# Performance work log

Measured on AMD Instinct MI355X. Metric: run time of the kernel, lower is better.

The kernel has to match this reference:

```python
import jax, jax.numpy as jnp
import numpy as np

D = 768      # hidden size (hardcoded in module)
H = 8        # MHA heads
DH = D // H  # head dim = 96
SLOPE = 0.01 # LeakyReLU default negative slope
NEG = -1e9


def _leaky(x):
    return jnp.where(x >= 0, x, SLOPE * x)


def setup_inputs() -> dict:
    key = jax.random.key(0)
    ks = jax.random.split(key, 20)
    B, S, T, C, L = 32, 2048, 64, 512, 16
    seq = jax.random.normal(ks[0], (B, S, D), dtype=jnp.float32)
    tab_ids = jax.random.randint(ks[1], (B, T, L), 0, S, dtype=jnp.int32)
    col_ids = jax.random.randint(ks[2], (B, C, L), 0, S, dtype=jnp.int32)
    # contiguous column->table assignment (8 cols/table), mirrors cumulative
    # slicing by column_number_in_each_table and keeps every table non-empty
    t_of_c = jnp.broadcast_to(jnp.repeat(jnp.arange(T, dtype=jnp.int32), C // T), (B, C))
    g = lambda k, sh: (jax.random.normal(k, sh, dtype=jnp.float32) * 0.02)
    return {
        "sequence_embeddings": seq,
        "table_token_ids": tab_ids,
        "column_token_ids": col_ids,
        "table_of_column": t_of_c,
        "W_tab_pool": g(ks[3], (D, D)), "b_tab_pool": g(ks[4], (D,)),
        "W_col_pool": g(ks[5], (D, D)), "b_col_pool": g(ks[6], (D,)),
        "in_proj_w": g(ks[7], (3 * D, D)), "in_proj_b": g(ks[8], (3 * D,)),
        "out_proj_w": g(ks[9], (D, D)), "out_proj_b": g(ks[10], (D,)),
        "W_t1": g(ks[11], (D, 256)), "b_t1": g(ks[12], (256,)),
        "W_t2": g(ks[13], (256, 2)), "b_t2": g(ks[14], (2,)),
        "W_c1": g(ks[15], (D, 256)), "b_c1": g(ks[16], (256,)),
        "W_c2": g(ks[17], (256, 2)), "b_c2": g(ks[18], (2,)),
    }


def reference(sequence_embeddings, table_token_ids, column_token_ids, table_of_column,
              W_tab_pool, b_tab_pool, W_col_pool, b_col_pool,
              in_proj_w, in_proj_b, out_proj_w, out_proj_b,
              W_t1, b_t1, W_t2, b_t2, W_c1, b_c1, W_c2, b_c2):
    B, T = table_token_ids.shape[:2]
    C = column_token_ids.shape[1]
    bi = jnp.arange(B)[:, None, None]
    # ragged span sum-pooling (gather + segment sum)
    tab = sequence_embeddings[bi, table_token_ids].sum(axis=2)   # [B,T,D]
    col = sequence_embeddings[bi, column_token_ids].sum(axis=2)  # [B,C,D]
    tab = _leaky(tab @ W_tab_pool + b_tab_pool)
    col = _leaky(col @ W_col_pool + b_col_pool)
    # per-table cross-attention (table query over its own columns), batched + masked
    Wq, Wk, Wv = jnp.split(in_proj_w, 3, axis=0)
    bq, bk, bv = jnp.split(in_proj_b, 3, axis=0)
    q = (tab @ Wq.T + bq).reshape(B, T, H, DH)
    k = (col @ Wk.T + bk).reshape(B, C, H, DH)
    v = (col @ Wv.T + bv).reshape(B, C, H, DH)
    scores = jnp.einsum('bthd,bchd->bhtc', q, k) / jnp.sqrt(jnp.float32(DH))
    mask = table_of_column[:, None, None, :] == jnp.arange(T, dtype=table_of_column.dtype)[None, None, :, None]
    attn = jax.nn.softmax(jnp.where(mask, scores, NEG), axis=-1)
    ctx = jnp.einsum('bhtc,bchd->bthd', attn, v).reshape(B, T, D)
    tab = tab + (ctx @ out_proj_w.T + out_proj_b)
    tab = tab / jnp.maximum(jnp.linalg.norm(tab, axis=-1, keepdims=True), 1e-12)
    # classification heads (dropout in eval mode = identity)
    t_logits = _leaky(tab @ W_t1 + b_t1) @ W_t2 + b_t2  # [B,T,2]
    c_logits = _leaky(col @ W_c1 + b_c1) @ W_c2 + b_c2  # [B,C,2]
    return jnp.concatenate([t_logits, c_logits], axis=1)  # [B,T+C,2]
```

## Files before the change

### kernel.cpp

```cpp
#include <hip/hip_runtime.h>
#include <hip/hip_bf16.h>

constexpr int Bc = 32;
constexpr int Sc = 2048;
constexpr int Tc = 64;
constexpr int Cc = 512;
constexpr int Lc = 16;
constexpr int Dc = 768;
constexpr int Hc = 8;
constexpr int DHc = 96;

typedef __attribute__((ext_vector_type(4))) float f32x4;
typedef __attribute__((ext_vector_type(8))) short bf16x8;
typedef __hip_bfloat16 bf;

__device__ inline unsigned short f2bf(float f) {
  __hip_bfloat16 h = __float2bfloat16(f);
  return *reinterpret_cast<unsigned short*>(&h);
}
__device__ inline float us2f(unsigned short u) {
  return __uint_as_float(((unsigned)u) << 16);
}

#define GLDS16(gp, lp)                                                        \
  __builtin_amdgcn_global_load_lds(                                           \
      (const __attribute__((address_space(1))) void*)(gp),                    \
      (__attribute__((address_space(3))) void*)(lp), 16, 0, 0)

__device__ inline void transpose32(const float* __restrict__ in,
                                   bf* __restrict__ outp, int K, int N,
                                   int ti, float (*t)[33]) {
  int nx = N >> 5;
  int bx = (ti % nx) * 32, by = (ti / nx) * 32;
  int x = threadIdx.x & 31, y = threadIdx.x >> 5;
#pragma unroll
  for (int i = 0; i < 32; i += 8)
    t[y + i][x] = in[(size_t)(by + y + i) * N + bx + x];
  __syncthreads();
#pragma unroll
  for (int i = 0; i < 32; i += 8)
    outp[(size_t)(bx + y + i) * K + by + x] = __float2bfloat16(t[x][y + i]);
}

__global__ __launch_bounds__(256) void prep_kernel(
    const float* __restrict__ W_tab_pool, const float* __restrict__ W_col_pool,
    const float* __restrict__ W_t1, const float* __restrict__ W_c1,
    const float* __restrict__ in_proj_w, const float* __restrict__ out_proj_w,
    const float* __restrict__ b_t2, const float* __restrict__ b_c2,
    bf* __restrict__ wtab_t, bf* __restrict__ wcol_t, bf* __restrict__ wt1_t,
    bf* __restrict__ wc1_t, bf* __restrict__ winproj, bf* __restrict__ woutproj,
    float* __restrict__ outd) {
  __shared__ float t[32][33];
  int blk = blockIdx.x, tid = threadIdx.x;
  if (blk < 576) {
    transpose32(W_tab_pool, wtab_t, Dc, Dc, blk, t);
  } else if (blk < 1152) {
    transpose32(W_col_pool, wcol_t, Dc, Dc, blk - 576, t);
  } else if (blk < 1344) {
    transpose32(W_t1, wt1_t, Dc, 256, blk - 1152, t);
  } else if (blk < 1536) {
    transpose32(W_c1, wc1_t, Dc, 256, blk - 1344, t);
  } else if (blk < 3264) {
    int i = (blk - 1536) * 256 + tid;
    float4 v = reinterpret_cast<const float4*>(in_proj_w)[i];
    reinterpret_cast<ushort4*>(winproj)[i] =
        make_ushort4(f2bf(v.x), f2bf(v.y), f2bf(v.z), f2bf(v.w));
  } else if (blk < 3840) {
    int i = (blk - 3264) * 256 + tid;
    float4 v = reinterpret_cast<const float4*>(out_proj_w)[i];
    reinterpret_cast<ushort4*>(woutproj)[i] =
        make_ushort4(f2bf(v.x), f2bf(v.y), f2bf(v.z), f2bf(v.w));
  } else {
    int e = (blk - 3840) * 256 + tid;
    int i = e & 1;
    int r = (e >> 1) % (Tc + Cc);
    outd[e] = (r < Tc) ? b_t2[i] : b_c2[i];
  }
}

__global__ __launch_bounds__(256) void pool_kernel(
    const float* __restrict__ seq, const int* __restrict__ tab_ids,
    const int* __restrict__ col_ids, bf* __restrict__ tabp,
    bf* __restrict__ colp) {
  int swz = (blockIdx.x & 7) * 576 + (blockIdx.x >> 3);
  int w = threadIdx.x >> 6, l = threadIdx.x & 63;
  int row = swz * 4 + w;
  int b = row / (Tc + Cc), r = row % (Tc + Cc);
  const int* ids;
  bf* outp;
  if (r < Tc) {
    ids = tab_ids + ((size_t)b * Tc + r) * Lc;
    outp = tabp + ((size_t)b * Tc + r) * Dc;
  } else {
    int c = r - Tc;
    ids = col_ids + ((size_t)b * Cc + c) * Lc;
    outp = colp + ((size_t)b * Cc + c) * Dc;
  }
  float4 a0 = {0, 0, 0, 0}, a1 = {0, 0, 0, 0}, a2 = {0, 0, 0, 0};
#pragma unroll
  for (int tix = 0; tix < Lc; ++tix) {
    const float4* p =
        reinterpret_cast<const float4*>(seq + ((size_t)b * Sc + ids[tix]) * Dc);
    float4 v0 = p[l], v1 = p[l + 64], v2 = p[l + 128];
    a0.x += v0.x; a0.y += v0.y; a0.z += v0.z; a0.w += v0.w;
    a1.x += v1.x; a1.y += v1.y; a1.z += v1.z; a1.w += v1.w;
    a2.x += v2.x; a2.y += v2.y; a2.z += v2.z; a2.w += v2.w;
  }
  ushort4* ob = reinterpret_cast<ushort4*>(outp);
  ob[l] = make_ushort4(f2bf(a0.x), f2bf(a0.y), f2bf(a0.z), f2bf(a0.w));
  ob[l + 64] = make_ushort4(f2bf(a1.x), f2bf(a1.y), f2bf(a1.z), f2bf(a1.w));
  ob[l + 128] = make_ushort4(f2bf(a2.x), f2bf(a2.y), f2bf(a2.z), f2bf(a2.w));
}

template <int OUTMODE, bool LEAKY, int LOG2RPB>
__global__ __launch_bounds__(256) void gemm_bf16(
    const bf* __restrict__ A, const bf* __restrict__ Bt,
    const float* __restrict__ bias, bf* __restrict__ Obf,
    float* __restrict__ Of32, const float* __restrict__ w2,
    float* __restrict__ outd, int out_base, int M, int N, int K) {
  constexpr int BM = 128, BN = 128, BK = 64;
  __shared__ bf As[BM * BK];
  __shared__ bf Bs[BN * BK];
  int tid = threadIdx.x;
  int row0 = blockIdx.y * BM, col0 = blockIdx.x * BN;
  int w = tid >> 6, l = tid & 63;
  int wr = (w >> 1) * 64, wc = (w & 1) * 64;
  f32x4 acc[4][4];
#pragma unroll
  for (int m = 0; m < 4; ++m)
#pragma unroll
    for (int n = 0; n < 4; ++n) acc[m][n] = f32x4{0.f, 0.f, 0.f, 0.f};

  int srow = tid >> 3, skk = (tid & 7) * 8;
  const bf* gA = A + (size_t)(row0 + srow) * K + skk;
  const bf* gB = Bt + (size_t)(col0 + srow) * K + skk;
  char* lA = (char*)As + tid * 16;
  char* lB = (char*)Bs + tid * 16;
  int lr = l & 15, lk = (l >> 4) * 8;

  for (int k0 = 0; k0 < K; k0 += BK) {
#pragma unroll
    for (int c = 0; c < 4; ++c) {
      GLDS16(gA + k0 + (size_t)c * 32 * K, lA + c * 4096);
      GLDS16(gB + k0 + (size_t)c * 32 * K, lB + c * 4096);
    }
    __syncthreads();
    bf16x8 af[2][4], bfr[2][4];
#pragma unroll
    for (int ks = 0; ks < 2; ++ks) {
#pragma unroll
      for (int m = 0; m < 4; ++m)
        af[ks][m] = *reinterpret_cast<const bf16x8*>(
            &As[(wr + m * 16 + lr) * BK + ks * 32 + lk]);
#pragma unroll
      for (int n = 0; n < 4; ++n)
        bfr[ks][n] = *reinterpret_cast<const bf16x8*>(
            &Bs[(wc + n * 16 + lr) * BK + ks * 32 + lk]);
    }
#pragma unroll
    for (int ks = 0; ks < 2; ++ks)
#pragma unroll
      for (int m = 0; m < 4; ++m)
#pragma unroll
        for (int n = 0; n < 4; ++n)
          acc[m][n] = __builtin_amdgcn_mfma_f32_16x16x32_bf16(
              af[ks][m], bfr[ks][n], acc[m][n], 0, 0, 0);
    __syncthreads();
  }

  int colI = l & 15, rowb = (l >> 4) * 4;
  if (OUTMODE == 3) {
    float w20[4], w21[4], bv[4];
#pragma unroll
    for (int n = 0; n < 4; ++n) {
      int c = col0 + wc + n * 16 + colI;
      w20[n] = w2[c * 2];
      w21[n] = w2[c * 2 + 1];
      bv[n] = bias[c];
    }
    float p0[4][4], p1[4][4];
#pragma unroll
    for (int m = 0; m < 4; ++m)
#pragma unroll
      for (int j = 0; j < 4; ++j) { p0[m][j] = 0.f; p1[m][j] = 0.f; }
#pragma unroll
    for (int m = 0; m < 4; ++m)
#pragma unroll
      for (int n = 0; n < 4; ++n)
#pragma unroll
        for (int j = 0; j < 4; ++j) {
          float v = acc[m][n][j] + bv[n];
          v = v >= 0.f ? v : 0.01f * v;
          p0[m][j] += v * w20[n];
          p1[m][j] += v * w21[n];
        }
#pragma unroll
    for (int m = 0; m < 4; ++m)
#pragma unroll
      for (int j = 0; j < 4; ++j) {
#pragma unroll
        for (int msk = 1; msk <= 8; msk <<= 1) {
          p0[m][j] += __shfl_xor(p0[m][j], msk);
          p1[m][j] += __shfl_xor(p1[m][j], msk);
        }
      }
    if (colI == 0) {
#pragma unroll
      for (int m = 0; m < 4; ++m)
#pragma unroll
        for (int j = 0; j < 4; ++j) {
          int grow = row0 + wr + m * 16 + rowb + j;
          int bb = grow >> LOG2RPB;
          int rr = grow & ((1 << LOG2RPB) - 1);
          int orow = bb * (Tc + Cc) + out_base + rr;
          atomicAdd(&outd[(size_t)orow * 2], p0[m][j]);
          atomicAdd(&outd[(size_t)orow * 2 + 1], p1[m][j]);
        }
    }
    return;
  }
#pragma unroll
  for (int m = 0; m < 4; ++m) {
#pragma unroll
    for (int n = 0; n < 4; ++n) {
      int c = col0 + wc + n * 16 + colI;
      float bv = bias ? bias[c] : 0.f;
#pragma unroll
      for (int j = 0; j < 4; ++j) {
        int r = row0 + wr + m * 16 + rowb + j;
        float v = acc[m][n][j] + bv;
        if (LEAKY) v = v >= 0.f ? v : 0.01f * v;
        if (OUTMODE == 0 || OUTMODE == 2)
          Obf[(size_t)r * N + c] = __float2bfloat16(v);
        if (OUTMODE == 1 || OUTMODE == 2) Of32[(size_t)r * N + c] = v;
      }
    }
  }
}

__global__ __launch_bounds__(256) void bucket_kernel(
    const int* __restrict__ t_of_c, int* __restrict__ col_sorted,
    int* __restrict__ offs) {
  int b = blockIdx.x, tid = threadIdx.x;
  __shared__ int cnt[Tc];
  __shared__ int cur[Tc + 1];
  if (tid < Tc) cnt[tid] = 0;
  __syncthreads();
  for (int c = tid; c < Cc; c += 256) atomicAdd(&cnt[t_of_c[b * Cc + c]], 1);
  __syncthreads();
  if (tid == 0) {
    int off = 0;
    for (int t = 0; t < Tc; ++t) {
      cur[t] = off;
      off += cnt[t];
    }
    cur[Tc] = off;
  }
  __syncthreads();
  if (tid <= Tc) offs[b * (Tc + 1) + tid] = cur[tid];
  __syncthreads();
  for (int c = tid; c < Cc; c += 256) {
    int t = t_of_c[b * Cc + c];
    int pos = atomicAdd(&cur[t], 1);
    col_sorted[b * Cc + pos] = c;
  }
}

__global__ __launch_bounds__(256) void attn_kernel(
    const bf* __restrict__ q, const bf* __restrict__ kv,
    const int* __restrict__ col_sorted, const int* __restrict__ offs,
    bf* __restrict__ ctx) {
  int b = blockIdx.x / Tc;
  int t = blockIdx.x % Tc;
  __shared__ float pbuf[Hc][Cc];
  __shared__ float den[Hc];
  __shared__ int cols_s[Cc];
  int tid = threadIdx.x;
  int o0 = offs[b * (Tc + 1) + t];
  int n = offs[b * (Tc + 1) + t + 1] - o0;
  for (int i = tid; i < n; i += 256)
    cols_s[i] = col_sorted[(size_t)b * Cc + o0 + i];
  __syncthreads();
  int h = tid >> 5, l32 = tid & 31, g = l32 >> 3, i8 = l32 & 7;
  const float scale = 0.10206207261596577f;
  float q12[12];
  {
    const ushort* qp = (const ushort*)q + ((size_t)b * Tc + t) * Dc + h * DHc + i8 * 12;
    ushort4 u0 = *(const ushort4*)(qp);
    ushort4 u1 = *(const ushort4*)(qp + 4);
    ushort4 u2 = *(const ushort4*)(qp + 8);
    q12[0] = us2f(u0.x); q12[1] = us2f(u0.y); q12[2] = us2f(u0.z); q12[3] = us2f(u0.w);
    q12[4] = us2f(u1.x); q12[5] = us2f(u1.y); q12[6] = us2f(u1.z); q12[7] = us2f(u1.w);
    q12[8] = us2f(u2.x); q12[9] = us2f(u2.y); q12[10] = us2f(u2.z); q12[11] = us2f(u2.w);
  }
  if (n > 0) {
    for (int jb = 0; jb < n; jb += 4) {
      int j = jb + g;
      float s = 0.f;
      if (j < n) {
        const ushort* kp =
            (const ushort*)kv + ((size_t)b * Cc + cols_s[j]) * 1536 + h * DHc + i8 * 12;
        ushort4 u0 = *(const ushort4*)(kp);
        ushort4 u1 = *(const ushort4*)(kp + 4);
        ushort4 u2 = *(const ushort4*)(kp + 8);
        s += q12[0] * us2f(u0.x) + q12[1] * us2f(u0.y) + q12[2] * us2f(u0.z) +
             q12[3] * us2f(u0.w);
        s += q12[4] * us2f(u1.x) + q12[5] * us2f(u1.y) + q12[6] * us2f(u1.z) +
             q12[7] * us2f(u1.w);
        s += q12[8] * us2f(u2.x) + q12[9] * us2f(u2.y) + q12[10] * us2f(u2.z) +
             q12[11] * us2f(u2.w);
      }
      s += __shfl_xor(s, 1);
      s += __shfl_xor(s, 2);
      s += __shfl_xor(s, 4);
      if (j < n && i8 == 0) pbuf[h][j] = s * scale;
    }
  }
  __syncthreads();
  if (n > 0) {
    float lmax = -3.0e38f;
    for (int j = l32; j < n; j += 32) lmax = fmaxf(lmax, pbuf[h][j]);
#pragma unroll
    for (int m = 16; m >= 1; m >>= 1) lmax = fmaxf(lmax, __shfl_xor(lmax, m));
    float lsum = 0.f;
    for (int j = l32; j < n; j += 32) {
      float e = __expf(pbuf[h][j] - lmax);
      pbuf[h][j] = e;
      lsum += e;
    }
#pragma unroll
    for (int m = 16; m >= 1; m >>= 1) lsum += __shfl_xor(lsum, m);
    if (l32 == 0) den[h] = lsum;
  } else if (l32 == 0) {
    den[h] = (float)Cc;
  }
  __syncthreads();
  int ncols = n > 0 ? n : Cc;
  float a12[12];
#pragma unroll
  for (int d = 0; d < 12; ++d) a12[d] = 0.f;
  for (int jb = 0; jb < ncols; jb += 4) {
    int j = jb + g;
    if (j < ncols) {
      int cj = n > 0 ? cols_s[j] : j;
      float pw = n > 0 ? pbuf[h][j] : 1.f;
      const ushort* vp =
          (const ushort*)kv + ((size_t)b * Cc + cj) * 1536 + 768 + h * DHc + i8 * 12;
      ushort4 u0 = *(const ushort4*)(vp);
      ushort4 u1 = *(const ushort4*)(vp + 4);
      ushort4 u2 = *(const ushort4*)(vp + 8);
      a12[0] += pw * us2f(u0.x); a12[1] += pw * us2f(u0.y);
      a12[2] += pw * us2f(u0.z); a12[3] += pw * us2f(u0.w);
      a12[4] += pw * us2f(u1.x); a12[5] += pw * us2f(u1.y);
      a12[6] += pw * us2f(u1.z); a12[7] += pw * us2f(u1.w);
      a12[8] += pw * us2f(u2.x); a12[9] += pw * us2f(u2.y);
      a12[10] += pw * us2f(u2.z); a12[11] += pw * us2f(u2.w);
    }
  }
#pragma unroll
  for (int d = 0; d < 12; ++d) {
    a12[d] += __shfl_xor(a12[d], 8);
    a12[d] += __shfl_xor(a12[d], 16);
  }
  float inv = 1.0f / den[h];
  if (g == 0) {
    ushort* cp = (ushort*)ctx + ((size_t)b * Tc + t) * Dc + h * DHc + i8 * 12;
    ushort4 o0 = make_ushort4(f2bf(a12[0] * inv), f2bf(a12[1] * inv),
                              f2bf(a12[2] * inv), f2bf(a12[3] * inv));
    ushort4 o1 = make_ushort4(f2bf(a12[4] * inv), f2bf(a12[5] * inv),
                              f2bf(a12[6] * inv), f2bf(a12[7] * inv));
    ushort4 o2 = make_ushort4(f2bf(a12[8] * inv), f2bf(a12[9] * inv),
                              f2bf(a12[10] * inv), f2bf(a12[11] * inv));
    *(ushort4*)(cp) = o0;
    *(ushort4*)(cp + 4) = o1;
    *(ushort4*)(cp + 8) = o2;
  }
}

__global__ __launch_bounds__(256) void addnorm_kernel(
    const float* __restrict__ tab, const float* __restrict__ proj,
    bf* __restrict__ tabn) {
  int row = blockIdx.x;
  int tid = threadIdx.x;
  size_t base = (size_t)row * Dc;
  float x0 = tab[base + tid] + proj[base + tid];
  float x1 = tab[base + tid + 256] + proj[base + tid + 256];
  float x2 = tab[base + tid + 512] + proj[base + tid + 512];
  float ss = x0 * x0 + x1 * x1 + x2 * x2;
#pragma unroll
  for (int m = 32; m >= 1; m >>= 1) ss += __shfl_xor(ss, m);
  __shared__ float red[4];
  int wave = tid >> 6, lane = tid & 63;
  if (lane == 0) red[wave] = ss;
  __syncthreads();
  float total = red[0] + red[1] + red[2] + red[3];
  float sc = 1.0f / fmaxf(sqrtf(total), 1e-12f);
  tabn[base + tid] = __float2bfloat16(x0 * sc);
  tabn[base + tid + 256] = __float2bfloat16(x1 * sc);
  tabn[base + tid + 512] = __float2bfloat16(x2 * sc);
}

extern "C" void kernel_launch(void* const* d_in, const int* in_sizes, int n_in,
                              void* d_out, int out_size, void* d_ws,
                              size_t ws_size, hipStream_t stream) {
  const float* seq = (const float*)d_in[0];
  const int* tab_ids = (const int*)d_in[1];
  const int* col_ids = (const int*)d_in[2];
  const int* t_of_c = (const int*)d_in[3];
  const float* W_tab_pool = (const float*)d_in[4];
  const float* b_tab_pool = (const float*)d_in[5];
  const float* W_col_pool = (const float*)d_in[6];
  const float* b_col_pool = (const float*)d_in[7];
  const float* in_proj_w = (const float*)d_in[8];
  const float* in_proj_b = (const float*)d_in[9];
  const float* out_proj_w = (const float*)d_in[10];
  const float* out_proj_b = (const float*)d_in[11];
  const float* W_t1 = (const float*)d_in[12];
  const float* b_t1 = (const float*)d_in[13];
  const float* W_t2 = (const float*)d_in[14];
  const float* b_t2 = (const float*)d_in[15];
  const float* W_c1 = (const float*)d_in[16];
  const float* b_c1 = (const float*)d_in[17];
  const float* W_c2 = (const float*)d_in[18];
  const float* b_c2 = (const float*)d_in[19];
  float* out = (float*)d_out;

  char* p = (char*)d_ws;
  auto alloc = [&](size_t bytes) -> char* {
    char* r = p;
    p += (bytes + 255) & ~(size_t)255;
    return r;
  };
  const size_t nBT = (size_t)Bc * Tc;
  const size_t nBC = (size_t)Bc * Cc;
  bf* tabp = (bf*)alloc(nBT * Dc * 2);
  bf* colp = (bf*)alloc(nBC * Dc * 2);
  bf* tabb_bf = (bf*)alloc(nBT * Dc * 2);
  float* tabb_f = (float*)alloc(nBT * Dc * 4);
  bf* colb = (bf*)alloc(nBC * Dc * 2);
  bf* qb = (bf*)alloc(nBT * Dc * 2);
  bf* kvb = (bf*)alloc(nBC * 1536 * 2);
  bf* ctxb = (bf*)alloc(nBT * Dc * 2);
  float* projb = (float*)alloc(nBT * Dc * 4);
  bf* tabn = (bf*)alloc(nBT * Dc * 2);
  bf* wtab_t = (bf*)alloc((size_t)Dc * Dc * 2);
  bf* wcol_t = (bf*)alloc((size_t)Dc * Dc * 2);
  bf* winproj = (bf*)alloc((size_t)3 * Dc * Dc * 2);
  bf* woutproj = (bf*)alloc((size_t)Dc * Dc * 2);
  bf* wt1_t = (bf*)alloc((size_t)256 * Dc * 2);
  bf* wc1_t = (bf*)alloc((size_t)256 * Dc * 2);
  int* col_sorted = (int*)alloc(nBC * 4);
  int* offs = (int*)alloc((size_t)Bc * (Tc + 1) * 4);

  prep_kernel<<<3984, 256, 0, stream>>>(W_tab_pool, W_col_pool, W_t1, W_c1,
                                        in_proj_w, out_proj_w, b_t2, b_c2,
                                        wtab_t, wcol_t, wt1_t, wc1_t, winproj,
                                        woutproj, out);
  bucket_kernel<<<Bc, 256, 0, stream>>>(t_of_c, col_sorted, offs);
  pool_kernel<<<Bc * (Tc + Cc) / 4, 256, 0, stream>>>(seq, tab_ids, col_ids,
                                                      tabp, colp);
  gemm_bf16<2, true, 0><<<dim3(Dc / 128, nBT / 128), 256, 0, stream>>>(
      tabp, wtab_t, b_tab_pool, tabb_bf, tabb_f, nullptr, nullptr, 0, nBT, Dc,
      Dc);
  gemm_bf16<0, true, 0><<<dim3(Dc / 128, nBC / 128), 256, 0, stream>>>(
      colp, wcol_t, b_col_pool, colb, nullptr, nullptr, nullptr, 0, nBC, Dc,
      Dc);
  gemm_bf16<0, false, 0><<<dim3(Dc / 128, nBT / 128), 256, 0, stream>>>(
      tabb_bf, winproj, in_proj_b, qb, nullptr, nullptr, nullptr, 0, nBT, Dc,
      Dc);
  gemm_bf16<0, false, 0><<<dim3(1536 / 128, nBC / 128), 256, 0, stream>>>(
      colb, winproj + (size_t)Dc * Dc, in_proj_b + Dc, kvb, nullptr, nullptr,
      nullptr, 0, nBC, 1536, Dc);
  attn_kernel<<<Bc * Tc, 256, 0, stream>>>(qb, kvb, col_sorted, offs, ctxb);
  gemm_bf16<1, false, 0><<<dim3(Dc / 128, nBT / 128), 256, 0, stream>>>(
      ctxb, woutproj, out_proj_b, nullptr, projb, nullptr, nullptr, 0, nBT, Dc,
      Dc);
  addnorm_kernel<<<nBT, 256, 0, stream>>>(tabb_f, projb, tabn);
  gemm_bf16<3, true, 6><<<dim3(256 / 128, nBT / 128), 256, 0, stream>>>(
      tabn, wt1_t, b_t1, nullptr, nullptr, W_t2, out, 0, nBT, 256, Dc);
  gemm_bf16<3, true, 9><<<dim3(256 / 128, nBC / 128), 256, 0, stream>>>(
      colb, wc1_t, b_c1, nullptr, nullptr, W_c2, out, Tc, nBC, 256, Dc);
}
```

Baseline: 603.6 us.

## Pre-convert sequence to bf16 for pooling gathers and merge GEMM launches

Adds a pass in the prep kernel that converts the whole sequence tensor to bf16, so the pooling gathers read half the bytes. The bucket sort moves into prep as well. Independent GEMMs are merged into combined launches with swizzled block ids: the two pooling projections, then q/kv plus the column classification head. The GEMM core is de-templated, which removes compile-time specialization, and the full-tensor conversion adds a read and write of the whole sequence. Rounding inputs to bf16 before summation also slightly changes accuracy.

```diff
diff --git a/kernel.cpp b/kernel.cpp
--- a/kernel.cpp
+++ b/kernel.cpp
@@ -47,10 +47,14 @@
     const float* __restrict__ W_t1, const float* __restrict__ W_c1,
     const float* __restrict__ in_proj_w, const float* __restrict__ out_proj_w,
     const float* __restrict__ b_t2, const float* __restrict__ b_c2,
+    const float* __restrict__ seq, const int* __restrict__ t_of_c,
     bf* __restrict__ wtab_t, bf* __restrict__ wcol_t, bf* __restrict__ wt1_t,
     bf* __restrict__ wc1_t, bf* __restrict__ winproj, bf* __restrict__ woutproj,
-    float* __restrict__ outd) {
+    float* __restrict__ outd, ushort* __restrict__ seqb,
+    int* __restrict__ col_sorted, int* __restrict__ offs) {
   __shared__ float t[32][33];
+  __shared__ int cnt[Tc];
+  __shared__ int cur[Tc + 1];
   int blk = blockIdx.x, tid = threadIdx.x;
   if (blk < 576) {
     transpose32(W_tab_pool, wtab_t, Dc, Dc, blk, t);
@@ -70,24 +74,54 @@
     float4 v = reinterpret_cast<const float4*>(out_proj_w)[i];
     reinterpret_cast<ushort4*>(woutproj)[i] =
         make_ushort4(f2bf(v.x), f2bf(v.y), f2bf(v.z), f2bf(v.w));
-  } else {
+  } else if (blk < 3984) {
     int e = (blk - 3840) * 256 + tid;
     int i = e & 1;
     int r = (e >> 1) % (Tc + Cc);
     outd[e] = (r < Tc) ? b_t2[i] : b_c2[i];
+  } else if (blk < 28560) {
+    int i0 = (blk - 3984) * 512 + tid;
+    const float4* s4 = reinterpret_cast<const float4*>(seq);
+    ushort4* o4 = reinterpret_cast<ushort4*>(seqb);
+    float4 v = s4[i0];
+    o4[i0] = make_ushort4(f2bf(v.x), f2bf(v.y), f2bf(v.z), f2bf(v.w));
+    float4 v2 = s4[i0 + 256];
+    o4[i0 + 256] = make_ushort4(f2bf(v2.x), f2bf(v2.y), f2bf(v2.z), f2bf(v2.w));
+  } else {
+    int b = blk - 28560;
+    if (tid < Tc) cnt[tid] = 0;
+    __syncthreads();
+    for (int c = tid; c < Cc; c += 256) atomicAdd(&cnt[t_of_c[b * Cc + c]], 1);
+    __syncthreads();
+    if (tid == 0) {
+      int off = 0;
+      for (int tt = 0; tt < Tc; ++tt) {
+        cur[tt] = off;
+        off += cnt[tt];
+      }
+      cur[Tc] = off;
+    }
+    __syncthreads();
+    if (tid <= Tc) offs[b * (Tc + 1) + tid] = cur[tid];
+    __syncthreads();
+    for (int c = tid; c < Cc; c += 256) {
+      int tt = t_of_c[b * Cc + c];
+      int pos = atomicAdd(&cur[tt], 1);
+      col_sorted[b * Cc + pos] = c;
+    }
   }
 }
 
 __global__ __launch_bounds__(256) void pool_kernel(
-    const float* __restrict__ seq, const int* __restrict__ tab_ids,
-    const int* __restrict__ col_ids, bf* __restrict__ tabp,
-    bf* __restrict__ colp) {
+    const ushort* __restrict__ seqb, const int* __restrict__ tab_ids,
+    const int* __restrict__ col_ids, ushort* __restrict__ tabp,
+    ushort* __restrict__ colp) {
   int swz = (blockIdx.x & 7) * 576 + (blockIdx.x >> 3);
   int w = threadIdx.x >> 6, l = threadIdx.x & 63;
   int row = swz * 4 + w;
   int b = row / (Tc + Cc), r = row % (Tc + Cc);
   const int* ids;
-  bf* outp;
+  ushort* outp;
   if (r < Tc) {
     ids = tab_ids + ((size_t)b * Tc + r) * Lc;
     outp = tabp + ((size_t)b * Tc + r) * Dc;
@@ -96,33 +130,33 @@
     ids = col_ids + ((size_t)b * Cc + c) * Lc;
     outp = colp + ((size_t)b * Cc + c) * Dc;
   }
-  float4 a0 = {0, 0, 0, 0}, a1 = {0, 0, 0, 0}, a2 = {0, 0, 0, 0};
+  float a0[4] = {0, 0, 0, 0}, a1[4] = {0, 0, 0, 0}, a2[4] = {0, 0, 0, 0};
 #pragma unroll
   for (int tix = 0; tix < Lc; ++tix) {
-    const float4* p =
-        reinterpret_cast<const float4*>(seq + ((size_t)b * Sc + ids[tix]) * Dc);
-    float4 v0 = p[l], v1 = p[l + 64], v2 = p[l + 128];
-    a0.x += v0.x; a0.y += v0.y; a0.z += v0.z; a0.w += v0.w;
-    a1.x += v1.x; a1.y += v1.y; a1.z += v1.z; a1.w += v1.w;
-    a2.x += v2.x; a2.y += v2.y; a2.z += v2.z; a2.w += v2.w;
+    const ushort4* p =
+        reinterpret_cast<const ushort4*>(seqb + ((size_t)b * Sc + ids[tix]) * Dc);
+    ushort4 u0 = p[l], u1 = p[l + 64], u2 = p[l + 128];
+    a0[0] += us2f(u0.x); a0[1] += us2f(u0.y); a0[2] += us2f(u0.z); a0[3] += us2f(u0.w);
+    a1[0] += us2f(u1.x); a1[1] += us2f(u1.y); a1[2] += us2f(u1.z); a1[3] += us2f(u1.w);
+    a2[0] += us2f(u2.x); a2[1] += us2f(u2.y); a2[2] += us2f(u2.z); a2[3] += us2f(u2.w);
   }
   ushort4* ob = reinterpret_cast<ushort4*>(outp);
-  ob[l] = make_ushort4(f2bf(a0.x), f2bf(a0.y), f2bf(a0.z), f2bf(a0.w));
-  ob[l + 64] = make_ushort4(f2bf(a1.x), f2bf(a1.y), f2bf(a1.z), f2bf(a1.w));
-  ob[l + 128] = make_ushort4(f2bf(a2.x), f2bf(a2.y), f2bf(a2.z), f2bf(a2.w));
-}
-
-template <int OUTMODE, bool LEAKY, int LOG2RPB>
-__global__ __launch_bounds__(256) void gemm_bf16(
+  ob[l] = make_ushort4(f2bf(a0[0]), f2bf(a0[1]), f2bf(a0[2]), f2bf(a0[3]));
+  ob[l + 64] = make_ushort4(f2bf(a1[0]), f2bf(a1[1]), f2bf(a1[2]), f2bf(a1[3]));
+  ob[l + 128] = make_ushort4(f2bf(a2[0]), f2bf(a2[1]), f2bf(a2[2]), f2bf(a2[3]));
+}
+
+__device__ __forceinline__ void gemm_core(
     const bf* __restrict__ A, const bf* __restrict__ Bt,
     const float* __restrict__ bias, bf* __restrict__ Obf,
     float* __restrict__ Of32, const float* __restrict__ w2,
-    float* __restrict__ outd, int out_base, int M, int N, int K) {
-  constexpr int BM = 128, BN = 128, BK = 64;
+    float* __restrict__ outd, int out_base, int log2rpb, int bx, int by, int N,
+    int leaky, int outmode) {
+  constexpr int BM = 128, BN = 128, BK = 64, K = Dc;
   __shared__ bf As[BM * BK];
   __shared__ bf Bs[BN * BK];
   int tid = threadIdx.x;
-  int row0 = blockIdx.y * BM, col0 = blockIdx.x * BN;
+  int row0 = by * BM, col0 = bx * BN;
   int w = tid >> 6, l = tid & 63;
   int wr = (w >> 1) * 64, wc = (w & 1) * 64;
   f32x4 acc[4][4];
@@ -169,7 +203,7 @@
   }
 
   int colI = l & 15, rowb = (l >> 4) * 4;
-  if (OUTMODE == 3) {
+  if (outmode == 3) {
     float w20[4], w21[4], bv[4];
 #pragma unroll
     for (int n = 0; n < 4; ++n) {
@@ -210,8 +244,8 @@
 #pragma unroll
         for (int j = 0; j < 4; ++j) {
           int grow = row0 + wr + m * 16 + rowb + j;
-          int bb = grow >> LOG2RPB;
-          int rr = grow & ((1 << LOG2RPB) - 1);
+          int bb = grow >> log2rpb;
+          int rr = grow & ((1 << log2rpb) - 1);
           int orow = bb * (Tc + Cc) + out_base + rr;
           atomicAdd(&outd[(size_t)orow * 2], p0[m][j]);
           atomicAdd(&outd[(size_t)orow * 2 + 1], p1[m][j]);
@@ -229,41 +263,62 @@
       for (int j = 0; j < 4; ++j) {
         int r = row0 + wr + m * 16 + rowb + j;
         float v = acc[m][n][j] + bv;
-        if (LEAKY) v = v >= 0.f ? v : 0.01f * v;
-        if (OUTMODE == 0 || OUTMODE == 2)
-          Obf[(size_t)r * N + c] = __float2bfloat16(v);
-        if (OUTMODE == 1 || OUTMODE == 2) Of32[(size_t)r * N + c] = v;
+        if (leaky) v = v >= 0.f ? v : 0.01f * v;
+        if (outmode == 0 || outmode == 2) Obf[(size_t)r * N + c] = __float2bfloat16(v);
+        if (outmode == 1 || outmode == 2) Of32[(size_t)r * N + c] = v;
       }
     }
   }
 }
 
-__global__ __launch_bounds__(256) void bucket_kernel(
-    const int* __restrict__ t_of_c, int* __restrict__ col_sorted,
-    int* __restrict__ offs) {
-  int b = blockIdx.x, tid = threadIdx.x;
-  __shared__ int cnt[Tc];
-  __shared__ int cur[Tc + 1];
-  if (tid < Tc) cnt[tid] = 0;
-  __syncthreads();
-  for (int c = tid; c < Cc; c += 256) atomicAdd(&cnt[t_of_c[b * Cc + c]], 1);
-  __syncthreads();
-  if (tid == 0) {
-    int off = 0;
-    for (int t = 0; t < Tc; ++t) {
-      cur[t] = off;
-      off += cnt[t];
-    }
-    cur[Tc] = off;
-  }
-  __syncthreads();
-  if (tid <= Tc) offs[b * (Tc + 1) + tid] = cur[tid];
-  __syncthreads();
-  for (int c = tid; c < Cc; c += 256) {
-    int t = t_of_c[b * Cc + c];
-    int pos = atomicAdd(&cur[t], 1);
-    col_sorted[b * Cc + pos] = c;
-  }
+__global__ __launch_bounds__(256) void gemm_pools(
+    const bf* __restrict__ tabp, const bf* __restrict__ colp,
+    const bf* __restrict__ wtab_t, const bf* __restrict__ wcol_t,
+    const float* __restrict__ b_tab, const float* __restrict__ b_col,
+    bf* __restrict__ tabb_bf, float* __restrict__ tabb_f,
+    bf* __restrict__ colb) {
+  int id = (blockIdx.x & 7) * 108 + (blockIdx.x >> 3);
+  if (id < 96) {
+    gemm_core(tabp, wtab_t, b_tab, tabb_bf, tabb_f, nullptr, nullptr, 0, 0,
+              id % 6, id / 6, Dc, 1, 2);
+  } else {
+    int r = id - 96;
+    gemm_core(colp, wcol_t, b_col, colb, nullptr, nullptr, nullptr, 0, 0,
+              r % 6, r / 6, Dc, 1, 0);
+  }
+}
+
+__global__ __launch_bounds__(256) void gemm_qkvc(
+    const bf* __restrict__ tabb_bf, const bf* __restrict__ colb,
+    const bf* __restrict__ winproj, const float* __restrict__ in_proj_b,
+    const bf* __restrict__ wc1_t, const float* __restrict__ b_c1,
+    const float* __restrict__ W_c2, bf* __restrict__ qb, bf* __restrict__ kvb,
+    float* __restrict__ outd) {
+  int id = (blockIdx.x & 7) * 236 + (blockIdx.x >> 3);
+  if (id < 96) {
+    gemm_core(tabb_bf, winproj, in_proj_b, qb, nullptr, nullptr, nullptr, 0, 0,
+              id % 6, id / 6, Dc, 0, 0);
+  } else if (id < 1632) {
+    int r = id - 96;
+    gemm_core(colb, winproj + (size_t)Dc * Dc, in_proj_b + Dc, kvb, nullptr,
+              nullptr, nullptr, 0, 0, r % 12, r / 12, 1536, 0, 0);
+  } else {
+    int r = id - 1632;
+    gemm_core(colb, wc1_t, b_c1, nullptr, nullptr, W_c2, outd, Tc, 9, r % 2,
+              r / 2, 256, 1, 3);
+  }
+}
+
+__global__ __launch_bounds__(256) void gemm_single(
+    const bf* __restrict__ A, const bf* __restrict__ Bt,
+    const float* __restrict__ bias, bf* __restrict__ Obf,
+    float* __restrict__ Of32, const float* __restrict__ w2,
+    float* __restrict__ outd, int out_base, int log2rpb, int nbx, int N,
+    int leaky, int outmode) {
+  int chunk = gridDim.x >> 3;
+  int id = (blockIdx.x & 7) * chunk + (blockIdx.x >> 3);
+  gemm_core(A, Bt, bias, Obf, Of32, w2, outd, out_base, log2rpb, id % nbx,
+            id / nbx, N, leaky, outmode);
 }
 
 __global__ __launch_bounds__(256) void attn_kernel(
@@ -285,7 +340,8 @@
   const float scale = 0.10206207261596577f;
   float q12[12];
   {
-    const ushort* qp = (const ushort*)q + ((size_t)b * Tc + t) * Dc + h * DHc + i8 * 12;
+    const ushort* qp =
+        (const ushort*)q + ((size_t)b * Tc + t) * Dc + h * DHc + i8 * 12;
     ushort4 u0 = *(const ushort4*)(qp);
     ushort4 u1 = *(const ushort4*)(qp + 4);
     ushort4 u2 = *(const ushort4*)(qp + 8);
@@ -298,8 +354,8 @@
       int j = jb + g;
       float s = 0.f;
       if (j < n) {
-        const ushort* kp =
-            (const ushort*)kv + ((size_t)b * Cc + cols_s[j]) * 1536 + h * DHc + i8 * 12;
+        const ushort* kp = (const ushort*)kv +
+                           ((size_t)b * Cc + cols_s[j]) * 1536 + h * DHc + i8 * 12;
         ushort4 u0 = *(const ushort4*)(kp);
         ushort4 u1 = *(const ushort4*)(kp + 4);
         ushort4 u2 = *(const ushort4*)(kp + 8);
@@ -344,8 +400,8 @@
     if (j < ncols) {
       int cj = n > 0 ? cols_s[j] : j;
       float pw = n > 0 ? pbuf[h][j] : 1.f;
-      const ushort* vp =
-          (const ushort*)kv + ((size_t)b * Cc + cj) * 1536 + 768 + h * DHc + i8 * 12;
+      const ushort* vp = (const ushort*)kv + ((size_t)b * Cc + cj) * 1536 +
+                         768 + h * DHc + i8 * 12;
       ushort4 u0 = *(const ushort4*)(vp);
       ushort4 u1 = *(const ushort4*)(vp + 4);
       ushort4 u2 = *(const ushort4*)(vp + 8);
@@ -365,15 +421,12 @@
   float inv = 1.0f / den[h];
   if (g == 0) {
     ushort* cp = (ushort*)ctx + ((size_t)b * Tc + t) * Dc + h * DHc + i8 * 12;
-    ushort4 o0 = make_ushort4(f2bf(a12[0] * inv), f2bf(a12[1] * inv),
-                              f2bf(a12[2] * inv), f2bf(a12[3] * inv));
-    ushort4 o1 = make_ushort4(f2bf(a12[4] * inv), f2bf(a12[5] * inv),
-                              f2bf(a12[6] * inv), f2bf(a12[7] * inv));
-    ushort4 o2 = make_ushort4(f2bf(a12[8] * inv), f2bf(a12[9] * inv),
-                              f2bf(a12[10] * inv), f2bf(a12[11] * inv));
-    *(ushort4*)(cp) = o0;
-    *(ushort4*)(cp + 4) = o1;
-    *(ushort4*)(cp + 8) = o2;
+    *(ushort4*)(cp) = make_ushort4(f2bf(a12[0] * inv), f2bf(a12[1] * inv),
+                                   f2bf(a12[2] * inv), f2bf(a12[3] * inv));
+    *(ushort4*)(cp + 4) = make_ushort4(f2bf(a12[4] * inv), f2bf(a12[5] * inv),
+                                       f2bf(a12[6] * inv), f2bf(a12[7] * inv));
+    *(ushort4*)(cp + 8) = make_ushort4(f2bf(a12[8] * inv), f2bf(a12[9] * inv),
+                                       f2bf(a12[10] * inv), f2bf(a12[11] * inv));
   }
 }
 
@@ -433,6 +486,7 @@
   };
   const size_t nBT = (size_t)Bc * Tc;
   const size_t nBC = (size_t)Bc * Cc;
+  ushort* seqb = (ushort*)alloc((size_t)Bc * Sc * Dc * 2);
   bf* tabp = (bf*)alloc(nBT * Dc * 2);
   bf* colp = (bf*)alloc(nBC * Dc * 2);
   bf* tabb_bf = (bf*)alloc(nBT * Dc * 2);
@@ -452,32 +506,22 @@
   int* col_sorted = (int*)alloc(nBC * 4);
   int* offs = (int*)alloc((size_t)Bc * (Tc + 1) * 4);
 
-  prep_kernel<<<3984, 256, 0, stream>>>(W_tab_pool, W_col_pool, W_t1, W_c1,
-                                        in_proj_w, out_proj_w, b_t2, b_c2,
-                                        wtab_t, wcol_t, wt1_t, wc1_t, winproj,
-                                        woutproj, out);
-  bucket_kernel<<<Bc, 256, 0, stream>>>(t_of_c, col_sorted, offs);
-  pool_kernel<<<Bc * (Tc + Cc) / 4, 256, 0, stream>>>(seq, tab_ids, col_ids,
-                                                      tabp, colp);
-  gemm_bf16<2, true, 0><<<dim3(Dc / 128, nBT / 128), 256, 0, stream>>>(
-      tabp, wtab_t, b_tab_pool, tabb_bf, tabb_f, nullptr, nullptr, 0, nBT, Dc,
-      Dc);
-  gemm_bf16<0, true, 0><<<dim3(Dc / 128, nBC / 128), 256, 0, stream>>>(
-      colp, wcol_t, b_col_pool, colb, nullptr, nullptr, nullptr, 0, nBC, Dc,
-      Dc);
-  gemm_bf16<0, false, 0><<<dim3(Dc / 128, nBT / 128), 256, 0, stream>>>(
-      tabb_bf, winproj, in_proj_b, qb, nullptr, nullptr, nullptr, 0, nBT, Dc,
-      Dc);
-  gemm_bf16<0, false, 0><<<dim3(1536 / 128, nBC / 128), 256, 0, stream>>>(
-      colb, winproj + (size_t)Dc * Dc, in_proj_b + Dc, kvb, nullptr, nullptr,
-      nullptr, 0, nBC, 1536, Dc);
+  prep_kernel<<<28592, 256, 0, stream>>>(
+      W_tab_pool, W_col_pool, W_t1, W_c1, in_proj_w, out_proj_w, b_t2, b_c2,
+      seq, t_of_c, wtab_t, wcol_t, wt1_t, wc1_t, winproj, woutproj, out,
+      seqb, col_sorted, offs);
+  pool_kernel<<<Bc * (Tc + Cc) / 4, 256, 0, stream>>>(seqb, tab_ids, col_ids,
+                                                      (ushort*)tabp,
+                                                      (ushort*)colp);
+  gemm_pools<<<864, 256, 0, stream>>>(tabp, colp, wtab_t, wcol_t, b_tab_pool,
+                                      b_col_pool, tabb_bf, tabb_f, colb);
+  gemm_qkvc<<<1888, 256, 0, stream>>>(tabb_bf, colb, winproj, in_proj_b, wc1_t,
+                                      b_c1, W_c2, qb, kvb, out);
   attn_kernel<<<Bc * Tc, 256, 0, stream>>>(qb, kvb, col_sorted, offs, ctxb);
-  gemm_bf16<1, false, 0><<<dim3(Dc / 128, nBT / 128), 256, 0, stream>>>(
-      ctxb, woutproj, out_proj_b, nullptr, projb, nullptr, nullptr, 0, nBT, Dc,
-      Dc);
+  gemm_single<<<96, 256, 0, stream>>>(ctxb, woutproj, out_proj_b, nullptr,
+                                      projb, nullptr, nullptr, 0, 0, 6, Dc, 0,
+                                      1);
   addnorm_kernel<<<nBT, 256, 0, stream>>>(tabb_f, projb, tabn);
-  gemm_bf16<3, true, 6><<<dim3(256 / 128, nBT / 128), 256, 0, stream>>>(
-      tabn, wt1_t, b_t1, nullptr, nullptr, W_t2, out, 0, nBT, 256, Dc);
-  gemm_bf16<3, true, 9><<<dim3(256 / 128, nBC / 128), 256, 0, stream>>>(
-      colb, wc1_t, b_c1, nullptr, nullptr, W_c2, out, Tc, nBC, 256, Dc);
-}
+  gemm_single<<<32, 256, 0, stream>>>(tabn, wt1_t, b_t1, nullptr, nullptr,
+                                      W_t2, out, 0, 6, 2, 256, 1, 3);
+}
```

Measured after the change: 572.1 us. 1.06x faster.
